# Kernel optimization log

Hardware: AMD Instinct MI355X
Metric: run time of the kernel (lower is better)

Reference implementation:

```python
import jax, jax.numpy as jnp
import numpy as np

TAU = 0.05
BIG_POSITIVE = 1.0e10
COS_EPS = 1e-8  # torch F.cosine_similarity default eps


def setup_inputs() -> dict:
    key = jax.random.key(0)
    k1, k2 = jax.random.split(key)
    b, d = 4096, 1024
    return {
        "batch_feat1": jax.random.normal(k1, (b, d), dtype=jnp.float32),
        "batch_feat2": jax.random.normal(k2, (b, d), dtype=jnp.float32),
        "input_mask": jnp.zeros((b,), dtype=jnp.int32),
    }


def reference(batch_feat1, batch_feat2, input_mask):
    # concat the two views: (2b, d)
    feat = jnp.concatenate([batch_feat1, batch_feat2], axis=0)
    bs = feat.shape[0]
    half = bs // 2

    # cosine similarity = normalize (clamped norm, as in torch) then GEMM
    norm = jnp.maximum(jnp.linalg.norm(feat, axis=-1, keepdims=True), COS_EPS)
    n = feat / norm
    similarity = n @ n.T  # (2b, 2b)

    # mask out self-similarity on the diagonal
    eye = jnp.eye(bs, dtype=similarity.dtype)
    logits = similarity / TAU - eye * BIG_POSITIVE

    idx = jnp.arange(half)
    y_true = jnp.concatenate([idx + half, idx])  # positive pair indices

    # weighted cross entropy: weight[c] = 1 - input_mask[c] (per-class weight)
    weight = (1 - jnp.concatenate([input_mask, input_mask], axis=0)).astype(logits.dtype)
    logp = jax.nn.log_softmax(logits, axis=-1)
    per_example = -jnp.take_along_axis(logp, y_true[:, None], axis=1)[:, 0]
    w = weight[y_true]
    loss = jnp.sum(w * per_example) / jnp.sum(w)
    return (loss, logits, y_true)
```

## Files before the change

kernel.cpp:

```cpp
#include <hip/hip_runtime.h>
#include <math.h>

#define BS 8192
#define HALF 4096
#define DIM 1024
#define BIGP 1.0e10f
#define SQRT_TAU_INV 4.472135955f

typedef __attribute__((ext_vector_type(8))) short bf16x8;
typedef __attribute__((ext_vector_type(4))) float f32x4;

#define GLOAD_LDS16(g, l)                                              \
    __builtin_amdgcn_global_load_lds(                                  \
        (const __attribute__((address_space(1))) void*)(g),            \
        (__attribute__((address_space(3))) void*)(l), 16, 0, 0)

__device__ inline unsigned short f2bf(float f) {
    union { float f; unsigned int u; } c; c.f = f;
    unsigned int u = c.u;
    u += 0x7FFFu + ((u >> 16) & 1u);
    return (unsigned short)(u >> 16);
}

__global__ __launch_bounds__(256) void norm_kernel(const float* __restrict__ f1,
                                                   const float* __restrict__ f2,
                                                   unsigned short* __restrict__ nb) {
    const int row = blockIdx.x;
    const int t = threadIdx.x;
    const float* src = (row < HALF) ? (f1 + (size_t)row * DIM)
                                    : (f2 + (size_t)(row - HALF) * DIM);
    float4 v = reinterpret_cast<const float4*>(src)[t];
    float ss = v.x * v.x + v.y * v.y + v.z * v.z + v.w * v.w;
#pragma unroll
    for (int off = 32; off > 0; off >>= 1) ss += __shfl_down(ss, off, 64);
    __shared__ float red[4];
    if ((t & 63) == 0) red[t >> 6] = ss;
    __syncthreads();
    float tot = red[0] + red[1] + red[2] + red[3];
    float inv = SQRT_TAU_INV / fmaxf(sqrtf(tot), 1e-8f);
    ushort4 o;
    o.x = f2bf(v.x * inv);
    o.y = f2bf(v.y * inv);
    o.z = f2bf(v.z * inv);
    o.w = f2bf(v.w * inv);
    reinterpret_cast<ushort4*>(nb + (size_t)row * DIM)[t] = o;
}

#define BM 128
#define BN 128
#define BK 64

__global__ __launch_bounds__(256) void gemm_kernel(const unsigned short* __restrict__ nb,
                                                   float* __restrict__ logits,
                                                   float* __restrict__ psum,
                                                   float* __restrict__ targ) {
    __shared__ unsigned short As[BM][BK];
    __shared__ unsigned short Bs[BN][BK];

    const int t = threadIdx.x;
    const int lane = t & 63;
    const int wid = t >> 6;
    const int wr = wid >> 1;
    const int wc = wid & 1;
    const int lo = lane & 15;
    const int hi = lane >> 4;

    const int id = blockIdx.x;
    int bx = (int)((sqrtf(8.0f * (float)id + 1.0f) - 1.0f) * 0.5f);
    while ((bx + 1) * (bx + 2) / 2 <= id) ++bx;
    while (bx * (bx + 1) / 2 > id) --bx;
    const int by = id - bx * (bx + 1) / 2;
    const bool diag = (bx == by);

    const int rowBase = by * BM;
    const int colBase = bx * BN;

    f32x4 acc[4][4];
#pragma unroll
    for (int m = 0; m < 4; ++m)
#pragma unroll
        for (int n = 0; n < 4; ++n) {
            acc[m][n][0] = 0.f; acc[m][n][1] = 0.f;
            acc[m][n][2] = 0.f; acc[m][n][3] = 0.f;
        }

    const int srow = lane >> 3;
    const int skoff = (((lane & 7) ^ srow) << 3);
    const char* Abase = (const char*)&As[0][0];
    const char* Bbase = (const char*)&Bs[0][0];
    const int rswz = (lo & 7) << 4;

    for (int kt = 0; kt < DIM; kt += BK) {
#pragma unroll
        for (int i = 0; i < 4; ++i) {
            const int chunk = wid * 4 + i;
            const int r = chunk * 8 + srow;
            const unsigned short* gA = nb + (size_t)(rowBase + r) * DIM + kt + skoff;
            GLOAD_LDS16(gA, (char*)&As[0][0] + chunk * 1024);
            const unsigned short* gB = nb + (size_t)(colBase + r) * DIM + kt + skoff;
            GLOAD_LDS16(gB, (char*)&Bs[0][0] + chunk * 1024);
        }
        __syncthreads();

#pragma unroll
        for (int ks = 0; ks < BK; ks += 32) {
            bf16x8 a[4], b[4];
#pragma unroll
            for (int m = 0; m < 4; ++m) {
                const int rr = wr * 64 + m * 16 + lo;
                a[m] = *reinterpret_cast<const bf16x8*>(
                    Abase + rr * 128 + ((ks * 2 + hi * 16) ^ rswz));
            }
#pragma unroll
            for (int n = 0; n < 4; ++n) {
                const int rr = wc * 64 + n * 16 + lo;
                b[n] = *reinterpret_cast<const bf16x8*>(
                    Bbase + rr * 128 + ((ks * 2 + hi * 16) ^ rswz));
            }
#pragma unroll
            for (int m = 0; m < 4; ++m)
#pragma unroll
                for (int n = 0; n < 4; ++n)
                    acc[m][n] = __builtin_amdgcn_mfma_f32_16x16x32_bf16(a[m], b[n], acc[m][n], 0, 0, 0);
        }
        __syncthreads();
    }

    if (diag) {
#pragma unroll
        for (int m = 0; m < 4; ++m) {
            const int lr0 = wr * 64 + m * 16 + hi * 4;
#pragma unroll
            for (int n = 0; n < 4; ++n) {
                const int lc = wc * 64 + n * 16 + lo;
#pragma unroll
                for (int r = 0; r < 4; ++r)
                    if (lr0 + r == lc) acc[m][n][r] -= BIGP;
            }
        }
    }

    float sums[16];
    float psn[4] = {0.f, 0.f, 0.f, 0.f};
#pragma unroll
    for (int p = 0; p < 16; ++p) sums[p] = 0.f;

#pragma unroll
    for (int m = 0; m < 4; ++m) {
        const int trow0 = rowBase + wr * 64 + m * 16 + hi * 4;
#pragma unroll
        for (int n = 0; n < 4; ++n) {
            const int col = colBase + wc * 64 + n * 16 + lo;
#pragma unroll
            for (int r = 0; r < 4; ++r) {
                const int row = trow0 + r;
                const float v = acc[m][n][r];
                logits[(size_t)row * BS + col] = v;
                if (col == row + HALF) { targ[row] = v; targ[col] = v; }
                const float e = __expf(v - 20.0f);
                sums[m * 4 + r] += e;
                psn[n] += e;
            }
        }
    }

    if (!diag) {
#pragma unroll
        for (int m = 0; m < 4; ++m) {
            const int trow0 = rowBase + wr * 64 + m * 16 + hi * 4;
#pragma unroll
            for (int n = 0; n < 4; ++n) {
                const int col = colBase + wc * 64 + n * 16 + lo;
                *reinterpret_cast<f32x4*>(&logits[(size_t)col * BS + trow0]) = acc[m][n];
            }
        }
    }

    float sel = 0.f;
#pragma unroll
    for (int p = 0; p < 16; ++p) {
        float sv = sums[p];
        sv += __shfl_xor(sv, 1, 64);
        sv += __shfl_xor(sv, 2, 64);
        sv += __shfl_xor(sv, 4, 64);
        sv += __shfl_xor(sv, 8, 64);
        sel = (lo == p) ? sv : sel;
    }
    psum[(size_t)(2 * bx + wc) * BS + rowBase + wr * 64 + (lo >> 2) * 16 + hi * 4 + (lo & 3)] = sel;

    if (!diag) {
#pragma unroll
        for (int n = 0; n < 4; ++n) {
            psn[n] += __shfl_xor(psn[n], 16, 64);
            psn[n] += __shfl_xor(psn[n], 32, 64);
        }
        const float cw = (hi == 0) ? psn[0] : (hi == 1) ? psn[1]
                       : (hi == 2) ? psn[2] : psn[3];
        psum[(size_t)(2 * by + wr) * BS + colBase + wc * 64 + hi * 16 + lo] = cw;
    }
}

__global__ __launch_bounds__(256) void reduce_rows_kernel(const float* __restrict__ psum,
                                                          const float* __restrict__ targ,
                                                          const int* __restrict__ mask,
                                                          float* __restrict__ partials,
                                                          float* __restrict__ ytrue_out) {
    const int t = threadIdx.x;
    const int row = blockIdx.x * 256 + t;

    float total = 0.f;
#pragma unroll 8
    for (int cb = 0; cb < 128; ++cb) total += psum[(size_t)cb * BS + row];

    const float pe = -(targ[row] - 20.0f - logf(total));
    const float w = 1.0f - (float)mask[row & (HALF - 1)];
    ytrue_out[row] = (float)((row < HALF) ? row + HALF : row - HALF);

    float a = w * pe, b = w;
#pragma unroll
    for (int off = 32; off > 0; off >>= 1) {
        a += __shfl_down(a, off, 64);
        b += __shfl_down(b, off, 64);
    }
    __shared__ float ra[4], rb[4];
    if ((t & 63) == 0) { ra[t >> 6] = a; rb[t >> 6] = b; }
    __syncthreads();
    if (t == 0) {
        partials[blockIdx.x] = ra[0] + ra[1] + ra[2] + ra[3];
        partials[32 + blockIdx.x] = rb[0] + rb[1] + rb[2] + rb[3];
    }
}

__global__ void loss_kernel(const float* __restrict__ partials,
                            float* __restrict__ loss_out) {
    if (threadIdx.x == 0) {
        float A = 0.f, B = 0.f;
        for (int i = 0; i < 32; ++i) { A += partials[i]; B += partials[32 + i]; }
        loss_out[0] = A / B;
    }
}

extern "C" void kernel_launch(void* const* d_in, const int* in_sizes, int n_in,
                              void* d_out, int out_size, void* d_ws, size_t ws_size,
                              hipStream_t stream) {
    const float* f1 = (const float*)d_in[0];
    const float* f2 = (const float*)d_in[1];
    const int* mask = (const int*)d_in[2];
    float* out = (float*)d_out;

    unsigned short* nb = (unsigned short*)d_ws;
    float* psum = (float*)((char*)d_ws + (size_t)BS * DIM * 2);
    float* targ = psum + (size_t)128 * BS;
    float* partials = targ + BS;
    float* logits = out + 1;
    float* ytrue_out = out + 1 + (size_t)BS * BS;

    norm_kernel<<<BS, 256, 0, stream>>>(f1, f2, nb);

    const int ntri = (BS / BM) * (BS / BM + 1) / 2;
    gemm_kernel<<<ntri, 256, 0, stream>>>(nb, logits, psum, targ);

    reduce_rows_kernel<<<BS / 256, 256, 0, stream>>>(psum, targ, mask, partials, ytrue_out);
    loss_kernel<<<1, 64, 0, stream>>>(partials, out);
}
```

Before: 172.9 us.

## Stage GEMM epilogue through LDS for coalesced logits stores and row sums

The GEMM epilogue now writes the accumulator tile into a padded shared-memory buffer, aliased over the A/B tiles, in four passes: two row halves and two transposed halves. It then reads it back so each thread writes contiguous float4 logits rows for both the tile and its mirrored transpose. Row exp-sums are computed per full 128-column tile, which halves the psum layout and changes the reduce kernel's indexing to match. The aim is to replace scattered scalar and strided transposed global stores with coalesced vector writes, at the cost of extra barriers and LDS traffic in the epilogue.

```diff
diff --git a/kernel.cpp b/kernel.cpp
--- a/kernel.cpp
+++ b/kernel.cpp
@@ -49,13 +49,16 @@
 #define BM 128
 #define BN 128
 #define BK 64
+#define TLD 133
 
 __global__ __launch_bounds__(256) void gemm_kernel(const unsigned short* __restrict__ nb,
                                                    float* __restrict__ logits,
                                                    float* __restrict__ psum,
                                                    float* __restrict__ targ) {
-    __shared__ unsigned short As[BM][BK];
-    __shared__ unsigned short Bs[BN][BK];
+    __shared__ union SM {
+        struct { unsigned short A[BM][BK]; unsigned short B[BN][BK]; } s;
+        float T[64][TLD];
+    } sm;
 
     const int t = threadIdx.x;
     const int lane = t & 63;
@@ -86,8 +89,8 @@
 
     const int srow = lane >> 3;
     const int skoff = (((lane & 7) ^ srow) << 3);
-    const char* Abase = (const char*)&As[0][0];
-    const char* Bbase = (const char*)&Bs[0][0];
+    const char* Abase = (const char*)&sm.s.A[0][0];
+    const char* Bbase = (const char*)&sm.s.B[0][0];
     const int rswz = (lo & 7) << 4;
 
     for (int kt = 0; kt < DIM; kt += BK) {
@@ -96,9 +99,9 @@
             const int chunk = wid * 4 + i;
             const int r = chunk * 8 + srow;
             const unsigned short* gA = nb + (size_t)(rowBase + r) * DIM + kt + skoff;
-            GLOAD_LDS16(gA, (char*)&As[0][0] + chunk * 1024);
+            GLOAD_LDS16(gA, (char*)&sm.s.A[0][0] + chunk * 1024);
             const unsigned short* gB = nb + (size_t)(colBase + r) * DIM + kt + skoff;
-            GLOAD_LDS16(gB, (char*)&Bs[0][0] + chunk * 1024);
+            GLOAD_LDS16(gB, (char*)&sm.s.B[0][0] + chunk * 1024);
         }
         __syncthreads();
 
@@ -140,63 +143,63 @@
         }
     }
 
-    float sums[16];
-    float psn[4] = {0.f, 0.f, 0.f, 0.f};
-#pragma unroll
-    for (int p = 0; p < 16; ++p) sums[p] = 0.f;
-
-#pragma unroll
-    for (int m = 0; m < 4; ++m) {
-        const int trow0 = rowBase + wr * 64 + m * 16 + hi * 4;
-#pragma unroll
-        for (int n = 0; n < 4; ++n) {
-            const int col = colBase + wc * 64 + n * 16 + lo;
-#pragma unroll
-            for (int r = 0; r < 4; ++r) {
-                const int row = trow0 + r;
-                const float v = acc[m][n][r];
-                logits[(size_t)row * BS + col] = v;
-                if (col == row + HALF) { targ[row] = v; targ[col] = v; }
-                const float e = __expf(v - 20.0f);
-                sums[m * 4 + r] += e;
-                psn[n] += e;
-            }
-        }
-    }
-
-    if (!diag) {
-#pragma unroll
-        for (int m = 0; m < 4; ++m) {
-            const int trow0 = rowBase + wr * 64 + m * 16 + hi * 4;
-#pragma unroll
-            for (int n = 0; n < 4; ++n) {
-                const int col = colBase + wc * 64 + n * 16 + lo;
-                *reinterpret_cast<f32x4*>(&logits[(size_t)col * BS + trow0]) = acc[m][n];
-            }
-        }
-    }
-
-    float sel = 0.f;
-#pragma unroll
-    for (int p = 0; p < 16; ++p) {
-        float sv = sums[p];
-        sv += __shfl_xor(sv, 1, 64);
-        sv += __shfl_xor(sv, 2, 64);
-        sv += __shfl_xor(sv, 4, 64);
-        sv += __shfl_xor(sv, 8, 64);
-        sel = (lo == p) ? sv : sel;
-    }
-    psum[(size_t)(2 * bx + wc) * BS + rowBase + wr * 64 + (lo >> 2) * 16 + hi * 4 + (lo & 3)] = sel;
-
-    if (!diag) {
-#pragma unroll
-        for (int n = 0; n < 4; ++n) {
-            psn[n] += __shfl_xor(psn[n], 16, 64);
-            psn[n] += __shfl_xor(psn[n], 32, 64);
-        }
-        const float cw = (hi == 0) ? psn[0] : (hi == 1) ? psn[1]
-                       : (hi == 2) ? psn[2] : psn[3];
-        psum[(size_t)(2 * by + wr) * BS + colBase + wc * 64 + hi * 16 + lo] = cw;
+#pragma unroll
+    for (int h = 0; h < 4; ++h) {
+        __syncthreads();
+        if (h < 2) {
+            if (wr == h) {
+#pragma unroll
+                for (int m = 0; m < 4; ++m)
+#pragma unroll
+                    for (int n = 0; n < 4; ++n)
+#pragma unroll
+                        for (int r = 0; r < 4; ++r)
+                            sm.T[m * 16 + hi * 4 + r][wc * 64 + n * 16 + lo] = acc[m][n][r];
+            }
+        } else {
+            if (wc == h - 2) {
+#pragma unroll
+                for (int m = 0; m < 4; ++m)
+#pragma unroll
+                    for (int n = 0; n < 4; ++n)
+#pragma unroll
+                        for (int r = 0; r < 4; ++r)
+                            sm.T[n * 16 + lo][wr * 64 + m * 16 + hi * 4 + r] = acc[m][n][r];
+            }
+        }
+        __syncthreads();
+
+        const bool tp = (h >= 2);
+        if (tp && diag) continue;
+        const int h2 = tp ? h - 2 : h;
+
+#pragma unroll
+        for (int sweep = 0; sweep < 8; ++sweep) {
+            const int idx = sweep * 256 + t;
+            const int rl = idx >> 5;
+            const int c4 = idx & 31;
+            const f32x4 w = *reinterpret_cast<const f32x4*>(&sm.T[rl][c4 * 4]);
+            float es = __expf(w[0] - 20.f) + __expf(w[1] - 20.f)
+                     + __expf(w[2] - 20.f) + __expf(w[3] - 20.f);
+            es += __shfl_xor(es, 1, 64);
+            es += __shfl_xor(es, 2, 64);
+            es += __shfl_xor(es, 4, 64);
+            es += __shfl_xor(es, 8, 64);
+            es += __shfl_xor(es, 16, 64);
+            if (!tp) {
+                const int row = rowBase + h2 * 64 + rl;
+                const int gc0 = colBase + c4 * 4;
+                *reinterpret_cast<f32x4*>(&logits[(size_t)row * BS + gc0]) = w;
+#pragma unroll
+                for (int q = 0; q < 4; ++q)
+                    if (gc0 + q == row + HALF) { targ[row] = w[q]; targ[row + HALF] = w[q]; }
+                if (c4 == 0) psum[(size_t)bx * BS + row] = es;
+            } else {
+                const int grow = colBase + h2 * 64 + rl;
+                *reinterpret_cast<f32x4*>(&logits[(size_t)grow * BS + rowBase + c4 * 4]) = w;
+                if (c4 == 0) psum[(size_t)(64 + by) * BS + grow] = es;
+            }
+        }
     }
 }
 
@@ -207,10 +210,11 @@
                                                           float* __restrict__ ytrue_out) {
     const int t = threadIdx.x;
     const int row = blockIdx.x * 256 + t;
+    const int rb = row >> 7;
 
     float total = 0.f;
-#pragma unroll 8
-    for (int cb = 0; cb < 128; ++cb) total += psum[(size_t)cb * BS + row];
+    for (int cb = rb; cb < 64; ++cb) total += psum[(size_t)cb * BS + row];
+    for (int cb = 0; cb < rb; ++cb) total += psum[(size_t)(64 + cb) * BS + row];
 
     const float pe = -(targ[row] - 20.0f - logf(total));
     const float w = 1.0f - (float)mask[row & (HALF - 1)];
@@ -222,12 +226,12 @@
         a += __shfl_down(a, off, 64);
         b += __shfl_down(b, off, 64);
     }
-    __shared__ float ra[4], rb[4];
-    if ((t & 63) == 0) { ra[t >> 6] = a; rb[t >> 6] = b; }
+    __shared__ float ra[4], rb_[4];
+    if ((t & 63) == 0) { ra[t >> 6] = a; rb_[t >> 6] = b; }
     __syncthreads();
     if (t == 0) {
         partials[blockIdx.x] = ra[0] + ra[1] + ra[2] + ra[3];
-        partials[32 + blockIdx.x] = rb[0] + rb[1] + rb[2] + rb[3];
+        partials[32 + blockIdx.x] = rb_[0] + rb_[1] + rb_[2] + rb_[3];
     }
 }
 
```

Result: slower. 208.4 us (+20.6%).

## Enlarge GEMM tiles to 256x256 with double-buffered LDS pipeline

Applied to the files above, without the earlier changes.

Doubles the symmetric GEMM tile to 256x256 with 8 waves per block, and double-buffers the LDS staging so global-to-LDS loads for tile k+2 overlap the MFMA work on tile k. It also raises MFMA priority around the compute blocks and reworks the partial-sum layout and row reduction to match the new tile shape. The goal is to cut global load traffic per output and hide load latency behind compute. In exchange it uses about 128KB of LDS per block, and 128 accumulator floats per thread under a (512,2) launch bound risk register spilling and lower occupancy.

```diff
diff --git a/kernel.cpp b/kernel.cpp
--- a/kernel.cpp
+++ b/kernel.cpp
@@ -6,6 +6,8 @@
 #define DIM 1024
 #define BIGP 1.0e10f
 #define SQRT_TAU_INV 4.472135955f
+#define BK 64
+#define NT (DIM / BK)
 
 typedef __attribute__((ext_vector_type(8))) short bf16x8;
 typedef __attribute__((ext_vector_type(4))) float f32x4;
@@ -46,22 +48,18 @@
     reinterpret_cast<ushort4*>(nb + (size_t)row * DIM)[t] = o;
 }
 
-#define BM 128
-#define BN 128
-#define BK 64
-
-__global__ __launch_bounds__(256) void gemm_kernel(const unsigned short* __restrict__ nb,
-                                                   float* __restrict__ logits,
-                                                   float* __restrict__ psum,
-                                                   float* __restrict__ targ) {
-    __shared__ unsigned short As[BM][BK];
-    __shared__ unsigned short Bs[BN][BK];
+__global__ __launch_bounds__(512, 2) void gemm_kernel(const unsigned short* __restrict__ nb,
+                                                      float* __restrict__ logits,
+                                                      float* __restrict__ psum,
+                                                      float* __restrict__ targ) {
+    __shared__ unsigned short As[2][256][BK];
+    __shared__ unsigned short Bs[2][256][BK];
 
     const int t = threadIdx.x;
     const int lane = t & 63;
     const int wid = t >> 6;
-    const int wr = wid >> 1;
-    const int wc = wid & 1;
+    const int wr = wid >> 2;
+    const int wcn = wid & 3;
     const int lo = lane & 15;
     const int hi = lane >> 4;
 
@@ -72,12 +70,12 @@
     const int by = id - bx * (bx + 1) / 2;
     const bool diag = (bx == by);
 
-    const int rowBase = by * BM;
-    const int colBase = bx * BN;
-
-    f32x4 acc[4][4];
-#pragma unroll
-    for (int m = 0; m < 4; ++m)
+    const int rowBase = by * 256;
+    const int colBase = bx * 256;
+
+    f32x4 acc[8][4];
+#pragma unroll
+    for (int m = 0; m < 8; ++m)
 #pragma unroll
         for (int n = 0; n < 4; ++n) {
             acc[m][n][0] = 0.f; acc[m][n][1] = 0.f;
@@ -86,53 +84,78 @@
 
     const int srow = lane >> 3;
     const int skoff = (((lane & 7) ^ srow) << 3);
-    const char* Abase = (const char*)&As[0][0];
-    const char* Bbase = (const char*)&Bs[0][0];
     const int rswz = (lo & 7) << 4;
 
-    for (int kt = 0; kt < DIM; kt += BK) {
-#pragma unroll
-        for (int i = 0; i < 4; ++i) {
-            const int chunk = wid * 4 + i;
-            const int r = chunk * 8 + srow;
-            const unsigned short* gA = nb + (size_t)(rowBase + r) * DIM + kt + skoff;
-            GLOAD_LDS16(gA, (char*)&As[0][0] + chunk * 1024);
-            const unsigned short* gB = nb + (size_t)(colBase + r) * DIM + kt + skoff;
-            GLOAD_LDS16(gB, (char*)&Bs[0][0] + chunk * 1024);
-        }
-        __syncthreads();
-
-#pragma unroll
-        for (int ks = 0; ks < BK; ks += 32) {
-            bf16x8 a[4], b[4];
-#pragma unroll
-            for (int m = 0; m < 4; ++m) {
-                const int rr = wr * 64 + m * 16 + lo;
-                a[m] = *reinterpret_cast<const bf16x8*>(
-                    Abase + rr * 128 + ((ks * 2 + hi * 16) ^ rswz));
-            }
+#define STAGE(kti, b) do {                                                       \
+    const int kt_ = (kti) * BK;                                                  \
+    _Pragma("unroll")                                                            \
+    for (int i_ = 0; i_ < 4; ++i_) {                                             \
+        const int chunk_ = wid * 4 + i_;                \
+        const int r_ = chunk_ * 8 + srow;                                        \
+        GLOAD_LDS16(nb + (size_t)(rowBase + r_) * DIM + kt_ + skoff,             \
+                    (char*)&As[b][0][0] + chunk_ * 1024);                        \
+        GLOAD_LDS16(nb + (size_t)(colBase + r_) * DIM + kt_ + skoff,             \
+                    (char*)&Bs[b][0][0] + chunk_ * 1024);                        \
+    } } while (0)
+
+#define COMPUTE(cur) do {                                                        \
+    const char* Ab = (const char*)&As[cur][0][0];                                \
+    const char* Bb = (const char*)&Bs[cur][0][0];                                \
+    bf16x8 bf[4][2];                                                             \
+    _Pragma("unroll")                                                            \
+    for (int n_ = 0; n_ < 4; ++n_)                                               \
+        _Pragma("unroll")                                                        \
+        for (int k2 = 0; k2 < 2; ++k2)                                           \
+            bf[n_][k2] = *reinterpret_cast<const bf16x8*>(                       \
+                Bb + (wcn * 64 + n_ * 16 + lo) * 128 + ((k2 * 64 + hi * 16) ^ rswz)); \
+    _Pragma("unroll")                                                            \
+    for (int q_ = 0; q_ < 4; ++q_) {                                             \
+        bf16x8 af[2][2];                                                         \
+        _Pragma("unroll")                                                        \
+        for (int mm = 0; mm < 2; ++mm)                                           \
+            _Pragma("unroll")                                                    \
+            for (int k2 = 0; k2 < 2; ++k2)                                       \
+                af[mm][k2] = *reinterpret_cast<const bf16x8*>(                   \
+                    Ab + (wr * 128 + (q_ * 2 + mm) * 16 + lo) * 128 +            \
+                         ((k2 * 64 + hi * 16) ^ rswz));                          \
+        __builtin_amdgcn_s_setprio(1);                                           \
+        _Pragma("unroll")                                                        \
+        for (int mm = 0; mm < 2; ++mm)                                           \
+            _Pragma("unroll")                                                    \
+            for (int n_ = 0; n_ < 4; ++n_)                                       \
+                _Pragma("unroll")                                                \
+                for (int k2 = 0; k2 < 2; ++k2)                                   \
+                    acc[q_ * 2 + mm][n_] = __builtin_amdgcn_mfma_f32_16x16x32_bf16( \
+                        af[mm][k2], bf[n_][k2], acc[q_ * 2 + mm][n_], 0, 0, 0);  \
+        __builtin_amdgcn_s_setprio(0);                                           \
+    } } while (0)
+
+    STAGE(0, 0);
+    STAGE(1, 1);
+
+    for (int kt = 0; kt < NT - 1; ++kt) {
+        const int cur = kt & 1;
+        asm volatile("s_waitcnt vmcnt(8)" ::: "memory");
+        __builtin_amdgcn_s_barrier();
+        asm volatile("" ::: "memory");
+        COMPUTE(cur);
+        asm volatile("" ::: "memory");
+        __builtin_amdgcn_s_barrier();
+        asm volatile("" ::: "memory");
+        if (kt + 2 < NT) STAGE(kt + 2, cur);
+    }
+    asm volatile("s_waitcnt vmcnt(0)" ::: "memory");
+    __builtin_amdgcn_s_barrier();
+    asm volatile("" ::: "memory");
+    COMPUTE((NT - 1) & 1);
+
+    if (diag) {
+#pragma unroll
+        for (int m = 0; m < 8; ++m) {
+            const int lr0 = wr * 128 + m * 16 + hi * 4;
 #pragma unroll
             for (int n = 0; n < 4; ++n) {
-                const int rr = wc * 64 + n * 16 + lo;
-                b[n] = *reinterpret_cast<const bf16x8*>(
-                    Bbase + rr * 128 + ((ks * 2 + hi * 16) ^ rswz));
-            }
-#pragma unroll
-            for (int m = 0; m < 4; ++m)
-#pragma unroll
-                for (int n = 0; n < 4; ++n)
-                    acc[m][n] = __builtin_amdgcn_mfma_f32_16x16x32_bf16(a[m], b[n], acc[m][n], 0, 0, 0);
-        }
-        __syncthreads();
-    }
-
-    if (diag) {
-#pragma unroll
-        for (int m = 0; m < 4; ++m) {
-            const int lr0 = wr * 64 + m * 16 + hi * 4;
-#pragma unroll
-            for (int n = 0; n < 4; ++n) {
-                const int lc = wc * 64 + n * 16 + lo;
+                const int lc = wcn * 64 + n * 16 + lo;
 #pragma unroll
                 for (int r = 0; r < 4; ++r)
                     if (lr0 + r == lc) acc[m][n][r] -= BIGP;
@@ -140,17 +163,17 @@
         }
     }
 
-    float sums[16];
+    float sums[32];
     float psn[4] = {0.f, 0.f, 0.f, 0.f};
 #pragma unroll
-    for (int p = 0; p < 16; ++p) sums[p] = 0.f;
-
-#pragma unroll
-    for (int m = 0; m < 4; ++m) {
-        const int trow0 = rowBase + wr * 64 + m * 16 + hi * 4;
+    for (int p = 0; p < 32; ++p) sums[p] = 0.f;
+
+#pragma unroll
+    for (int m = 0; m < 8; ++m) {
+        const int trow0 = rowBase + wr * 128 + m * 16 + hi * 4;
 #pragma unroll
         for (int n = 0; n < 4; ++n) {
-            const int col = colBase + wc * 64 + n * 16 + lo;
+            const int col = colBase + wcn * 64 + n * 16 + lo;
 #pragma unroll
             for (int r = 0; r < 4; ++r) {
                 const int row = trow0 + r;
@@ -166,17 +189,17 @@
 
     if (!diag) {
 #pragma unroll
-        for (int m = 0; m < 4; ++m) {
-            const int trow0 = rowBase + wr * 64 + m * 16 + hi * 4;
+        for (int m = 0; m < 8; ++m) {
+            const int trow0 = rowBase + wr * 128 + m * 16 + hi * 4;
 #pragma unroll
             for (int n = 0; n < 4; ++n) {
-                const int col = colBase + wc * 64 + n * 16 + lo;
+                const int col = colBase + wcn * 64 + n * 16 + lo;
                 *reinterpret_cast<f32x4*>(&logits[(size_t)col * BS + trow0]) = acc[m][n];
             }
         }
     }
 
-    float sel = 0.f;
+    float sel0 = 0.f, sel1 = 0.f;
 #pragma unroll
     for (int p = 0; p < 16; ++p) {
         float sv = sums[p];
@@ -184,9 +207,20 @@
         sv += __shfl_xor(sv, 2, 64);
         sv += __shfl_xor(sv, 4, 64);
         sv += __shfl_xor(sv, 8, 64);
-        sel = (lo == p) ? sv : sel;
-    }
-    psum[(size_t)(2 * bx + wc) * BS + rowBase + wr * 64 + (lo >> 2) * 16 + hi * 4 + (lo & 3)] = sel;
+        sel0 = (lo == p) ? sv : sel0;
+    }
+#pragma unroll
+    for (int p = 0; p < 16; ++p) {
+        float sv = sums[16 + p];
+        sv += __shfl_xor(sv, 1, 64);
+        sv += __shfl_xor(sv, 2, 64);
+        sv += __shfl_xor(sv, 4, 64);
+        sv += __shfl_xor(sv, 8, 64);
+        sel1 = (lo == p) ? sv : sel1;
+    }
+    const int base_r = rowBase + wr * 128 + (lo >> 2) * 16 + hi * 4 + (lo & 3);
+    psum[(size_t)(4 * bx + wcn) * BS + base_r] = sel0;
+    psum[(size_t)(4 * bx + wcn) * BS + base_r + 64] = sel1;
 
     if (!diag) {
 #pragma unroll
@@ -196,8 +230,10 @@
         }
         const float cw = (hi == 0) ? psn[0] : (hi == 1) ? psn[1]
                        : (hi == 2) ? psn[2] : psn[3];
-        psum[(size_t)(2 * by + wr) * BS + colBase + wc * 64 + hi * 16 + lo] = cw;
-    }
+        psum[(size_t)(128 + 2 * by + wr) * BS + colBase + wcn * 64 + hi * 16 + lo] = cw;
+    }
+#undef STAGE
+#undef COMPUTE
 }
 
 __global__ __launch_bounds__(256) void reduce_rows_kernel(const float* __restrict__ psum,
@@ -207,10 +243,11 @@
                                                           float* __restrict__ ytrue_out) {
     const int t = threadIdx.x;
     const int row = blockIdx.x * 256 + t;
+    const int rb = row >> 8;
 
     float total = 0.f;
-#pragma unroll 8
-    for (int cb = 0; cb < 128; ++cb) total += psum[(size_t)cb * BS + row];
+    for (int s = 4 * rb; s < 128; ++s) total += psum[(size_t)s * BS + row];
+    for (int s = 0; s < 2 * rb; ++s) total += psum[(size_t)(128 + s) * BS + row];
 
     const float pe = -(targ[row] - 20.0f - logf(total));
     const float w = 1.0f - (float)mask[row & (HALF - 1)];
@@ -222,12 +259,12 @@
         a += __shfl_down(a, off, 64);
         b += __shfl_down(b, off, 64);
     }
-    __shared__ float ra[4], rb[4];
-    if ((t & 63) == 0) { ra[t >> 6] = a; rb[t >> 6] = b; }
+    __shared__ float ra[4], rb_[4];
+    if ((t & 63) == 0) { ra[t >> 6] = a; rb_[t >> 6] = b; }
     __syncthreads();
     if (t == 0) {
         partials[blockIdx.x] = ra[0] + ra[1] + ra[2] + ra[3];
-        partials[32 + blockIdx.x] = rb[0] + rb[1] + rb[2] + rb[3];
+        partials[32 + blockIdx.x] = rb_[0] + rb_[1] + rb_[2] + rb_[3];
     }
 }
 
@@ -250,15 +287,15 @@
 
     unsigned short* nb = (unsigned short*)d_ws;
     float* psum = (float*)((char*)d_ws + (size_t)BS * DIM * 2);
-    float* targ = psum + (size_t)128 * BS;
+    float* targ = psum + (size_t)192 * BS;
     float* partials = targ + BS;
     float* logits = out + 1;
     float* ytrue_out = out + 1 + (size_t)BS * BS;
 
     norm_kernel<<<BS, 256, 0, stream>>>(f1, f2, nb);
 
-    const int ntri = (BS / BM) * (BS / BM + 1) / 2;
-    gemm_kernel<<<ntri, 256, 0, stream>>>(nb, logits, psum, targ);
+    const int ntri = 32 * 33 / 2;
+    gemm_kernel<<<ntri, 512, 0, stream>>>(nb, logits, psum, targ);
 
     reduce_rows_kernel<<<BS / 256, 256, 0, stream>>>(psum, targ, mask, partials, ytrue_out);
     loss_kernel<<<1, 64, 0, stream>>>(partials, out);
```

New measurement: 196.0 us. 13.4% more time.
